# Kernel tuning notes

Measured on AMD Instinct MI355X. Metric: run time of the kernel, lower is better.

Reference implementation:

```python
import jax, jax.numpy as jnp
import numpy as np

NUM_HEADS = 16
LN_EPS = 1e-5

def _gelu(x):
    return jax.nn.gelu(x, approximate=False)  # torch default GELU is exact (erf)

def setup_inputs() -> dict:
    key = jax.random.key(0)
    ks = jax.random.split(key, 12)
    B, S, E = 2, 2048, 1024
    H = E // 2
    s = lambda fan_in: 1.0 / np.sqrt(fan_in)
    inp = {
        "x": jax.random.normal(ks[0], (B, S, E), jnp.float32),
        "Wq": jax.random.normal(ks[1], (E, E), jnp.float32) * s(E),
        "bq": jnp.zeros((E,), jnp.float32),
        "Wk": jax.random.normal(ks[2], (E, E), jnp.float32) * s(E),
        "bk": jnp.zeros((E,), jnp.float32),
        "Wv": jax.random.normal(ks[3], (E, E), jnp.float32) * s(E),
        "bv": jnp.zeros((E,), jnp.float32),
        "Wo": jax.random.normal(ks[4], (E, E), jnp.float32) * s(E),
        "bo": jnp.zeros((E,), jnp.float32),
        "dp_w1": jax.random.normal(ks[5], (E, H), jnp.float32) * s(E),
        "dp_b1": jnp.zeros((H,), jnp.float32),
        "ln_g": jnp.ones((H,), jnp.float32),
        "ln_b": jnp.zeros((H,), jnp.float32),
        "dp_w2": jax.random.normal(ks[6], (H, 1), jnp.float32) * s(H),
        "dp_b2": jnp.zeros((1,), jnp.float32),
        "g_w1": jax.random.normal(ks[7], (1, 16), jnp.float32),
        "g_b1": jnp.zeros((16,), jnp.float32),
        "g_w2": jax.random.normal(ks[8], (16, 1), jnp.float32) * s(16),
        "g_b2": jnp.zeros((1,), jnp.float32),
    }
    return inp


def reference(x, Wq, bq, Wk, bk, Wv, bv, Wo, bo,
              dp_w1, dp_b1, ln_g, ln_b, dp_w2, dp_b2,
              g_w1, g_b1, g_w2, g_b2):
    B, S, E = x.shape
    Hn = NUM_HEADS
    Dh = E // Hn
    scale = Dh ** -0.5

    Q = (x @ Wq + bq).reshape(B, S, Hn, Dh)
    K = (x @ Wk + bk).reshape(B, S, Hn, Dh)
    V = (x @ Wv + bv).reshape(B, S, Hn, Dh)

    # (B, H, q, k)
    logits = jnp.einsum('bqhd,bkhd->bhqk', Q, K) * scale
    causal = jnp.tril(jnp.ones((S, S), bool))
    logits = jnp.where(causal, logits, -jnp.inf)
    attn = jax.nn.softmax(logits, axis=-1)

    # drift probe: Linear -> LayerNorm -> GELU -> Linear, squeeze -> (B, S)
    h = x @ dp_w1 + dp_b1
    mu = h.mean(-1, keepdims=True)
    var = ((h - mu) ** 2).mean(-1, keepdims=True)
    h = (h - mu) / jnp.sqrt(var + LN_EPS) * ln_g + ln_b
    drift = (_gelu(h) @ dp_w2 + dp_b2)[..., 0]

    # drift_to_gate: Linear(1,16) -> GELU -> Linear(16,1) -> Tanh -> (B, S)
    g = _gelu(drift[..., None] * g_w1[0] + g_b1)
    gate = jnp.tanh(g @ g_w2 + g_b2)[..., 0]  # (B, S), indexed by key position

    gated = attn * gate[:, None, None, :]  # dropout p=0 -> identity
    out = jnp.einsum('bhqk,bkhd->bqhd', gated, V).reshape(B, S, E)
    return out @ Wo + bo
```

## Files before the change

### kernel.cpp

```cpp
#include <hip/hip_runtime.h>
#include <math.h>
#include <stdint.h>

#define B_   2
#define S_   2048
#define E_   1024
#define NH   16
#define DH   64
#define HID  512
#define NCAT 3584
#define MTOK 4096

typedef unsigned short ushort_t;
typedef short  s16x8  __attribute__((ext_vector_type(8)));
typedef unsigned short us4 __attribute__((ext_vector_type(4)));
typedef float  f32x4  __attribute__((ext_vector_type(4)));

static constexpr float LN_EPS    = 1e-5f;
static constexpr float SCALE     = 0.125f;
static constexpr float INV_SQRT2 = 0.70710678118654752440f;

__device__ __forceinline__ float gelu_exact(float v) {
    return 0.5f * v * (1.0f + erff(v * INV_SQRT2));
}

__device__ __forceinline__ ushort_t f2bf(float f) {
    unsigned int u = __float_as_uint(f);
    unsigned int r = u + 0x7fffu + ((u >> 16) & 1u);
    return (ushort_t)(r >> 16);
}
__device__ __forceinline__ float bf2f(ushort_t s) {
    return __uint_as_float(((unsigned int)s) << 16);
}

__device__ __forceinline__ void stage16(const void* g, void* ldsbase) {
#if __has_builtin(__builtin_amdgcn_global_load_lds)
    __builtin_amdgcn_global_load_lds(
        (const __attribute__((address_space(1))) void*)g,
        (__attribute__((address_space(3))) void*)ldsbase, 16, 0, 0);
#else
    ((uint4*)ldsbase)[threadIdx.x & 63] = *(const uint4*)g;
#endif
}

__device__ __forceinline__ void xcd_swizzle(int gx, int gy, int& bx, int& by) {
    const int T = gx * gy;
    const int lin = blockIdx.y * gx + blockIdx.x;
    const int work = (lin & 7) * (T >> 3) + (lin >> 3);
    bx = work % gx;
    by = work / gx;
}

__global__ __launch_bounds__(256) void preproc_kernel(
    const float* __restrict__ x,
    const float* __restrict__ Wq, const float* __restrict__ Wk,
    const float* __restrict__ Wv, const float* __restrict__ Wo,
    const float* __restrict__ dpw1,
    const float* __restrict__ bq, const float* __restrict__ bk,
    const float* __restrict__ bv, const float* __restrict__ b1,
    ushort_t* __restrict__ xh, ushort_t* __restrict__ xl,
    ushort_t* __restrict__ bth, ushort_t* __restrict__ btl,
    ushort_t* __restrict__ woth, ushort_t* __restrict__ wotl,
    float* __restrict__ bcat)
{
    __shared__ float tile[32][33];
    int bid = blockIdx.x;
    const int t = threadIdx.x;

    if (bid < 1024) {
        int base = bid * 1024 + t;
        #pragma unroll
        for (int it = 0; it < 4; ++it) {
            int i = base + it * 256;
            float4 v = ((const float4*)x)[i];
            float vv[4] = {v.x, v.y, v.z, v.w};
            us4 h, l;
            #pragma unroll
            for (int j = 0; j < 4; ++j) {
                ushort_t hh = f2bf(vv[j]);
                h[j] = hh;
                l[j] = f2bf(vv[j] - bf2f(hh));
            }
            *(us4*)&xh[(size_t)i * 4] = h;
            *(us4*)&xl[(size_t)i * 4] = l;
        }
        return;
    }
    bid -= 1024;
    if (bid < 4608) {
        const float* W; ushort_t *th, *tl; int N, kx, ny;
        if (bid < 1024)      { W = Wq;   th = bth;                        tl = btl;                        N = 1024; kx = bid & 31; ny = bid >> 5; }
        else if (bid < 2048) { W = Wk;   th = bth + (size_t)1024 * E_;    tl = btl + (size_t)1024 * E_;    N = 1024; kx = (bid - 1024) & 31; ny = (bid - 1024) >> 5; }
        else if (bid < 3072) { W = Wv;   th = bth + (size_t)2048 * E_;    tl = btl + (size_t)2048 * E_;    N = 1024; kx = (bid - 2048) & 31; ny = (bid - 2048) >> 5; }
        else if (bid < 4096) { W = Wo;   th = woth;                       tl = wotl;                       N = 1024; kx = (bid - 3072) & 31; ny = (bid - 3072) >> 5; }
        else                 { W = dpw1; th = bth + (size_t)3072 * E_;    tl = btl + (size_t)3072 * E_;    N = 512;  kx = (bid - 4096) & 31; ny = (bid - 4096) >> 5; }

        const int k0 = kx * 32, n0 = ny * 32;
        const int r = t >> 3, c4 = (t & 7) * 4;
        float4 v = *(const float4*)&W[(size_t)(k0 + r) * N + n0 + c4];
        tile[r][c4 + 0] = v.x; tile[r][c4 + 1] = v.y;
        tile[r][c4 + 2] = v.z; tile[r][c4 + 3] = v.w;
        __syncthreads();
        us4 h, l;
        #pragma unroll
        for (int i = 0; i < 4; ++i) {
            float xv = tile[c4 + i][r];
            ushort_t hh = f2bf(xv);
            h[i] = hh;
            l[i] = f2bf(xv - bf2f(hh));
        }
        *(us4*)&th[(size_t)(n0 + r) * E_ + k0 + c4] = h;
        *(us4*)&tl[(size_t)(n0 + r) * E_ + k0 + c4] = l;
        return;
    }
    bid -= 4608;
    int i = bid * 256 + t;
    if (i >= NCAT) return;
    float v;
    if      (i < 1024) v = bq[i];
    else if (i < 2048) v = bk[i - 1024];
    else if (i < 3072) v = bv[i - 2048];
    else               v = b1[i - 3072];
    bcat[i] = v;
}

struct GemmCtx {
    int lane, w, wr, wc;
};

__device__ __forceinline__ void gemm_core(
    const ushort_t* __restrict__ Ah, const ushort_t* __restrict__ Al,
    const ushort_t* __restrict__ Bh, const ushort_t* __restrict__ Bl,
    int row0, int col0, int Kd,
    ushort_t* Ahs, ushort_t* Als, ushort_t* Bhs, ushort_t* Bls,
    f32x4 (&acc)[4][4], const GemmCtx& cx)
{
    const int lr = cx.lane >> 2;
    const int lc = (cx.lane & 3) * 8;

    for (int k0 = 0; k0 < Kd; k0 += 32) {
        #pragma unroll
        for (int ii = 0; ii < 2; ++ii) {
            const int r0 = (cx.w * 2 + ii) * 16;
            const size_t ga = (size_t)(row0 + r0 + lr) * Kd + k0 + lc;
            const size_t gb = (size_t)(col0 + r0 + lr) * Kd + k0 + lc;
            stage16(Ah + ga, &Ahs[r0 * 32]);
            stage16(Al + ga, &Als[r0 * 32]);
            stage16(Bh + gb, &Bhs[r0 * 32]);
            stage16(Bl + gb, &Bls[r0 * 32]);
        }
        __syncthreads();

        const int rA = cx.wr * 64 + (cx.lane & 15);
        const int rB = cx.wc * 64 + (cx.lane & 15);
        const int kq = (cx.lane >> 4) * 8;
        s16x8 fah[4], fal[4], fbh[4], fbl[4];
        #pragma unroll
        for (int i = 0; i < 4; ++i) {
            fah[i] = *(const s16x8*)&Ahs[(rA + i * 16) * 32 + kq];
            fal[i] = *(const s16x8*)&Als[(rA + i * 16) * 32 + kq];
            fbh[i] = *(const s16x8*)&Bhs[(rB + i * 16) * 32 + kq];
            fbl[i] = *(const s16x8*)&Bls[(rB + i * 16) * 32 + kq];
        }
        __builtin_amdgcn_s_setprio(1);
        #pragma unroll
        for (int i = 0; i < 4; ++i)
            #pragma unroll
            for (int j = 0; j < 4; ++j) {
                acc[i][j] = __builtin_amdgcn_mfma_f32_16x16x32_bf16(fah[i], fbh[j], acc[i][j], 0, 0, 0);
                acc[i][j] = __builtin_amdgcn_mfma_f32_16x16x32_bf16(fah[i], fbl[j], acc[i][j], 0, 0, 0);
                acc[i][j] = __builtin_amdgcn_mfma_f32_16x16x32_bf16(fal[i], fbh[j], acc[i][j], 0, 0, 0);
            }
        __builtin_amdgcn_s_setprio(0);
        __syncthreads();
    }
}

__global__ __launch_bounds__(256) void mfma_gemm_qkvh_kernel(
    const ushort_t* __restrict__ Ah, const ushort_t* __restrict__ Al,
    const ushort_t* __restrict__ Bh, const ushort_t* __restrict__ Bl,
    const float* __restrict__ bias,
    ushort_t* __restrict__ Qh, ushort_t* __restrict__ Ql,
    ushort_t* __restrict__ Kh, ushort_t* __restrict__ Kl,
    float* __restrict__ v32, float* __restrict__ h32)
{
    __shared__ __align__(16) ushort_t Ahs[128 * 32];
    __shared__ __align__(16) ushort_t Als[128 * 32];
    __shared__ __align__(16) ushort_t Bhs[128 * 32];
    __shared__ __align__(16) ushort_t Bls[128 * 32];

    int bx, by;
    xcd_swizzle(28, 32, bx, by);
    const int row0 = by * 128, col0 = bx * 128;

    GemmCtx cx;
    cx.lane = threadIdx.x & 63;
    cx.w    = threadIdx.x >> 6;
    cx.wr   = cx.w >> 1; cx.wc = cx.w & 1;

    f32x4 acc[4][4] = {};
    gemm_core(Ah, Al, Bh, Bl, row0, col0, E_, Ahs, Als, Bhs, Bls, acc, cx);

    const int crow = row0 + cx.wr * 64 + ((cx.lane >> 4) * 4);
    const int ccol0 = col0 + cx.wc * 64 + (cx.lane & 15);

    #pragma unroll
    for (int j = 0; j < 4; ++j) {
        const int gcol = ccol0 + j * 16;
        const float bv = bias[gcol];
        #pragma unroll
        for (int i = 0; i < 4; ++i)
            #pragma unroll
            for (int r = 0; r < 4; ++r) {
                const int row = crow + i * 16 + r;
                float val = acc[i][j][r] + bv;
                if (gcol < 1024) {
                    val *= SCALE;
                    ushort_t hi = f2bf(val);
                    Qh[(size_t)row * 1024 + gcol] = hi;
                    Ql[(size_t)row * 1024 + gcol] = f2bf(val - bf2f(hi));
                } else if (gcol < 2048) {
                    ushort_t hi = f2bf(val);
                    Kh[(size_t)row * 1024 + gcol - 1024] = hi;
                    Kl[(size_t)row * 1024 + gcol - 1024] = f2bf(val - bf2f(hi));
                } else if (gcol < 3072) {
                    v32[(size_t)row * 1024 + gcol - 2048] = val;
                } else {
                    h32[(size_t)row * 512 + gcol - 3072] = val;
                }
            }
    }
}

__global__ __launch_bounds__(256) void mfma_gemm_kernel(
    const ushort_t* __restrict__ Ah, const ushort_t* __restrict__ Al,
    const ushort_t* __restrict__ Bh, const ushort_t* __restrict__ Bl,
    const float* __restrict__ bias,
    float* __restrict__ C, int N, int Kd)
{
    __shared__ __align__(16) ushort_t Ahs[128 * 32];
    __shared__ __align__(16) ushort_t Als[128 * 32];
    __shared__ __align__(16) ushort_t Bhs[128 * 32];
    __shared__ __align__(16) ushort_t Bls[128 * 32];

    int bx, by;
    xcd_swizzle(gridDim.x, gridDim.y, bx, by);
    const int row0 = by * 128, col0 = bx * 128;

    GemmCtx cx;
    cx.lane = threadIdx.x & 63;
    cx.w    = threadIdx.x >> 6;
    cx.wr   = cx.w >> 1; cx.wc = cx.w & 1;

    f32x4 acc[4][4] = {};
    gemm_core(Ah, Al, Bh, Bl, row0, col0, Kd, Ahs, Als, Bhs, Bls, acc, cx);

    const int crow = row0 + cx.wr * 64 + ((cx.lane >> 4) * 4);
    const int ccol = col0 + cx.wc * 64 + (cx.lane & 15);
    #pragma unroll
    for (int j = 0; j < 4; ++j) {
        const float bv = bias[ccol + j * 16];
        #pragma unroll
        for (int i = 0; i < 4; ++i)
            #pragma unroll
            for (int r = 0; r < 4; ++r)
                C[(size_t)(crow + i * 16 + r) * N + ccol + j * 16] = acc[i][j][r] + bv;
    }
}

__global__ __launch_bounds__(256) void ln_gate_kernel(
    const float* __restrict__ h32,
    const float* __restrict__ lng, const float* __restrict__ lnb,
    const float* __restrict__ w2,  const float* __restrict__ b2,
    const float* __restrict__ gw1, const float* __restrict__ gb1,
    const float* __restrict__ gw2, const float* __restrict__ gb2,
    float* __restrict__ gate)
{
    const int row  = blockIdx.x * 4 + (threadIdx.x >> 6);
    const int lane = threadIdx.x & 63;
    const float* h = h32 + (size_t)row * 512;

    float4 a = *(const float4*)&h[lane * 4];
    float4 b = *(const float4*)&h[256 + lane * 4];
    float va[8] = {a.x, a.y, a.z, a.w, b.x, b.y, b.z, b.w};

    float sum = 0.f, sq = 0.f;
    #pragma unroll
    for (int j = 0; j < 8; ++j) { sum += va[j]; sq += va[j] * va[j]; }
    #pragma unroll
    for (int o = 1; o < 64; o <<= 1) {
        sum += __shfl_xor(sum, o);
        sq  += __shfl_xor(sq,  o);
    }
    const float mu  = sum * (1.f / HID);
    const float inv = 1.f / sqrtf(sq * (1.f / HID) - mu * mu + LN_EPS);

    float4 g0 = *(const float4*)&lng[lane * 4];
    float4 g1 = *(const float4*)&lng[256 + lane * 4];
    float4 o0 = *(const float4*)&lnb[lane * 4];
    float4 o1 = *(const float4*)&lnb[256 + lane * 4];
    float4 w0 = *(const float4*)&w2[lane * 4];
    float4 w1 = *(const float4*)&w2[256 + lane * 4];
    float gg[8] = {g0.x, g0.y, g0.z, g0.w, g1.x, g1.y, g1.z, g1.w};
    float bb[8] = {o0.x, o0.y, o0.z, o0.w, o1.x, o1.y, o1.z, o1.w};
    float ww[8] = {w0.x, w0.y, w0.z, w0.w, w1.x, w1.y, w1.z, w1.w};

    float part = 0.f;
    #pragma unroll
    for (int j = 0; j < 8; ++j) {
        float nx = (va[j] - mu) * inv * gg[j] + bb[j];
        part += gelu_exact(nx) * ww[j];
    }
    #pragma unroll
    for (int o = 1; o < 64; o <<= 1) part += __shfl_xor(part, o);

    if (lane == 0) {
        float drift = part + b2[0];
        float gacc = gb2[0];
        #pragma unroll
        for (int i = 0; i < 16; ++i) {
            float tt = fmaf(drift, gw1[i], gb1[i]);
            gacc = fmaf(gelu_exact(tt), gw2[i], gacc);
        }
        gate[row] = tanhf(gacc);
    }
}

__global__ __launch_bounds__(256) void v_transpose_kernel(
    const float* __restrict__ v32, const float* __restrict__ gate,
    ushort_t* __restrict__ Vth, ushort_t* __restrict__ Vtl)
{
    __shared__ float T[64 * 68];
    const int kt = blockIdx.x, bh = blockIdx.y;
    const int b = bh >> 4, h = bh & 15;
    const int tid = threadIdx.x;

    #pragma unroll
    for (int it = 0; it < 4; ++it) {
        int idx = tid + it * 256;
        int tokr = idx >> 4, f4 = idx & 15;
        int tok = b * S_ + kt * 64 + tokr;
        float g = gate[tok];
        float4 v = *(const float4*)&v32[(size_t)tok * 1024 + h * 64 + f4 * 4];
        T[(f4 * 4 + 0) * 68 + tokr] = v.x * g;
        T[(f4 * 4 + 1) * 68 + tokr] = v.y * g;
        T[(f4 * 4 + 2) * 68 + tokr] = v.z * g;
        T[(f4 * 4 + 3) * 68 + tokr] = v.w * g;
    }
    __syncthreads();

    const int d = tid >> 2, t0 = (tid & 3) * 16;
    const size_t obase = (size_t)bh * 64 * S_ + (size_t)d * S_ + kt * 64 + t0;
    s16x8 h8[2], l8[2];
    #pragma unroll
    for (int u = 0; u < 16; ++u) {
        float f = T[d * 68 + t0 + u];
        ushort_t hh = f2bf(f);
        h8[u >> 3][u & 7] = (short)hh;
        l8[u >> 3][u & 7] = (short)f2bf(f - bf2f(hh));
    }
    *(s16x8*)&Vth[obase]     = h8[0];
    *(s16x8*)&Vth[obase + 8] = h8[1];
    *(s16x8*)&Vtl[obase]     = l8[0];
    *(s16x8*)&Vtl[obase + 8] = l8[1];
}

__global__ __launch_bounds__(512, 4) void attn_mfma_kernel(
    const ushort_t* __restrict__ Qh, const ushort_t* __restrict__ Ql,
    const ushort_t* __restrict__ Kh, const ushort_t* __restrict__ Kl,
    const ushort_t* __restrict__ Vth, const ushort_t* __restrict__ Vtl,
    ushort_t* __restrict__ ch, ushort_t* __restrict__ cl)
{
    __shared__ __align__(16) ushort_t Khs[64 * 72], Kls[64 * 72];
    __shared__ __align__(16) ushort_t Vhs[64 * 72], Vls[64 * 72];
    __shared__ __align__(16) unsigned int Ph[8 * 16 * 32];
    __shared__ __align__(16) unsigned int Pl[8 * 16 * 32];

    const int tid  = threadIdx.x;
    const int lane = tid & 63;
    const int w    = tid >> 6;
    const int g    = lane >> 4;
    const int c    = lane & 15;

    const int lin  = blockIdx.y * 16 + blockIdx.x;
    const int work = (lin & 7) * 64 + (lin >> 3);
    const int bh   = work >> 4;
    const int qt   = 15 - (work & 15);
    const int b    = bh >> 4, h = bh & 15;
    const int q0   = qt * 128;

    const size_t qkb = (size_t)b * S_ * 1024 + h * 64;
    const size_t vtb = (size_t)bh * 64 * S_;

    const int qwave = q0 + w * 16;

    const size_t qrow = qkb + (size_t)(qwave + c) * 1024;
    s16x8 qfh[2], qfl[2];
    qfh[0] = *(const s16x8*)&Qh[qrow + g * 8];
    qfh[1] = *(const s16x8*)&Qh[qrow + 32 + g * 8];
    qfl[0] = *(const s16x8*)&Ql[qrow + g * 8];
    qfl[1] = *(const s16x8*)&Ql[qrow + 32 + g * 8];

    f32x4 o4[4] = {};
    float m = -INFINITY, l = 0.f;

    #define PIDX(c_, kp_) ((w << 9) + ((c_) << 5) + ((kp_) ^ (((c_) & 7) << 2)))

    const int srow = tid >> 3, ssl = tid & 7;

    s16x8 pkh, pkl, pvh, pvl;
    pkh = *(const s16x8*)&Kh [qkb + (size_t)srow * 1024 + ssl * 8];
    pkl = *(const s16x8*)&Kl [qkb + (size_t)srow * 1024 + ssl * 8];
    pvh = *(const s16x8*)&Vth[vtb + (size_t)srow * S_ + ssl * 8];
    pvl = *(const s16x8*)&Vtl[vtb + (size_t)srow * S_ + ssl * 8];

    const int ktmax = 2 * qt + 1;

    for (int kt = 0; kt <= ktmax; ++kt) {
        const int k0 = kt * 64;
        *(s16x8*)&Khs[srow * 72 + ssl * 8] = pkh;
        *(s16x8*)&Kls[srow * 72 + ssl * 8] = pkl;
        *(s16x8*)&Vhs[srow * 72 + ssl * 8] = pvh;
        *(s16x8*)&Vls[srow * 72 + ssl * 8] = pvl;
        __syncthreads();

        if (kt < ktmax) {
            const int kn = k0 + 64;
            pkh = *(const s16x8*)&Kh [qkb + (size_t)(kn + srow) * 1024 + ssl * 8];
            pkl = *(const s16x8*)&Kl [qkb + (size_t)(kn + srow) * 1024 + ssl * 8];
            pvh = *(const s16x8*)&Vth[vtb + (size_t)srow * S_ + kn + ssl * 8];
            pvl = *(const s16x8*)&Vtl[vtb + (size_t)srow * S_ + kn + ssl * 8];
        }

        if (k0 <= qwave + 15) {
            f32x4 s4[4] = {};
            __builtin_amdgcn_s_setprio(1);
            #pragma unroll
            for (int j = 0; j < 4; ++j)
                #pragma unroll
                for (int ks = 0; ks < 2; ++ks) {
                    s16x8 kfh = *(const s16x8*)&Khs[(c + j * 16) * 72 + ks * 32 + g * 8];
                    s16x8 kfl = *(const s16x8*)&Kls[(c + j * 16) * 72 + ks * 32 + g * 8];
                    s4[j] = __builtin_amdgcn_mfma_f32_16x16x32_bf16(kfh, qfh[ks], s4[j], 0, 0, 0);
                    s4[j] = __builtin_amdgcn_mfma_f32_16x16x32_bf16(kfh, qfl[ks], s4[j], 0, 0, 0);
                    s4[j] = __builtin_amdgcn_mfma_f32_16x16x32_bf16(kfl, qfh[ks], s4[j], 0, 0, 0);
                }
            __builtin_amdgcn_s_setprio(0);

            if (k0 + 63 > qwave) {
                #pragma unroll
                for (int j = 0; j < 4; ++j)
                    #pragma unroll
                    for (int r = 0; r < 4; ++r)
                        if (k0 + j * 16 + g * 4 + r > qwave + c)
                            s4[j][r] = -INFINITY;
            }

            float pmax = -INFINITY;
            #pragma unroll
            for (int j = 0; j < 4; ++j)
                #pragma unroll
                for (int r = 0; r < 4; ++r) pmax = fmaxf(pmax, s4[j][r]);
            pmax = fmaxf(pmax, __shfl_xor(pmax, 16));
            pmax = fmaxf(pmax, __shfl_xor(pmax, 32));

            const bool nomax = __all(pmax <= m);
            const float mn = nomax ? m : fmaxf(m, pmax);

            float ps = 0.f;
            #pragma unroll
            for (int j = 0; j < 4; ++j)
                #pragma unroll
                for (int r = 0; r < 4; ++r) {
                    float p = __expf(s4[j][r] - mn);
                    s4[j][r] = p;
                    ps += p;
                }
            ps += __shfl_xor(ps, 16);
            ps += __shfl_xor(ps, 32);

            if (nomax) {
                l += ps;
            } else {
                float corr = (m == -INFINITY) ? 0.f : __expf(m - mn);
                l = l * corr + ps;
                m = mn;
                #pragma unroll
                for (int r = 0; r < 4; ++r) {
                    int src = ((g << 4) | (g * 4 + r)) << 2;
                    float cr = __int_as_float(
                        __builtin_amdgcn_ds_bpermute(src, __float_as_int(corr)));
                    #pragma unroll
                    for (int j = 0; j < 4; ++j) o4[j][r] *= cr;
                }
            }

            #pragma unroll
            for (int j = 0; j < 4; ++j)
                #pragma unroll
                for (int p = 0; p < 2; ++p) {
                    float e  = s4[j][2 * p];
                    float od = s4[j][2 * p + 1];
                    unsigned int hi2, lo2;
                    asm volatile("v_cvt_pk_bf16_f32 %0, %1, %2"
                                 : "=v"(hi2) : "v"(e), "v"(od));
                    float ef = __uint_as_float(hi2 << 16);
                    float of = __uint_as_float(hi2 & 0xffff0000u);
                    float el = e - ef, ol = od - of;
                    asm volatile("v_cvt_pk_bf16_f32 %0, %1, %2"
                                 : "=v"(lo2) : "v"(el), "v"(ol));
                    const int kp = j * 8 + g * 2 + p;
                    Ph[PIDX(c, kp)] = hi2;
                    Pl[PIDX(c, kp)] = lo2;
                }
            asm volatile("s_waitcnt lgkmcnt(0)" ::: "memory");
            __builtin_amdgcn_sched_barrier(0);

            union U4 { uint4 u; s16x8 v; };
            s16x8 pah[2], pal[2];
            #pragma unroll
            for (int ks = 0; ks < 2; ++ks) {
                U4 a, bb;
                a.u  = *(const uint4*)&Ph[PIDX(c, ks * 16 + g * 4)];
                bb.u = *(const uint4*)&Pl[PIDX(c, ks * 16 + g * 4)];
                pah[ks] = a.v;
                pal[ks] = bb.v;
            }

            __builtin_amdgcn_s_setprio(1);
            #pragma unroll
            for (int j = 0; j < 4; ++j)
                #pragma unroll
                for (int ks = 0; ks < 2; ++ks) {
                    s16x8 vfh = *(const s16x8*)&Vhs[(c + j * 16) * 72 + ks * 32 + g * 8];
                    s16x8 vfl = *(const s16x8*)&Vls[(c + j * 16) * 72 + ks * 32 + g * 8];
                    o4[j] = __builtin_amdgcn_mfma_f32_16x16x32_bf16(pah[ks], vfh, o4[j], 0, 0, 0);
                    o4[j] = __builtin_amdgcn_mfma_f32_16x16x32_bf16(pah[ks], vfl, o4[j], 0, 0, 0);
                    o4[j] = __builtin_amdgcn_mfma_f32_16x16x32_bf16(pal[ks], vfh, o4[j], 0, 0, 0);
                }
            __builtin_amdgcn_s_setprio(0);
        }
        __syncthreads();
    }

    float inv[4];
    #pragma unroll
    for (int r = 0; r < 4; ++r) {
        int src = ((g << 4) | (g * 4 + r)) << 2;
        float lb = __int_as_float(
            __builtin_amdgcn_ds_bpermute(src, __float_as_int(l)));
        inv[r] = 1.f / lb;
    }
    #pragma unroll
    for (int j = 0; j < 4; ++j)
        #pragma unroll
        for (int r = 0; r < 4; ++r) {
            float val = o4[j][r] * inv[r];
            int tok = b * S_ + qwave + g * 4 + r;
            int col = h * 64 + c + j * 16;
            ushort_t hi = f2bf(val);
            ch[(size_t)tok * 1024 + col] = hi;
            cl[(size_t)tok * 1024 + col] = f2bf(val - bf2f(hi));
        }
    #undef PIDX
}

extern "C" void kernel_launch(void* const* d_in, const int* in_sizes, int n_in,
                              void* d_out, int out_size, void* d_ws, size_t ws_size,
                              hipStream_t stream)
{
    const float* x    = (const float*)d_in[0];
    const float* Wq   = (const float*)d_in[1];  const float* bq   = (const float*)d_in[2];
    const float* Wk   = (const float*)d_in[3];  const float* bk   = (const float*)d_in[4];
    const float* Wv   = (const float*)d_in[5];  const float* bv   = (const float*)d_in[6];
    const float* Wo   = (const float*)d_in[7];  const float* bo   = (const float*)d_in[8];
    const float* dpw1 = (const float*)d_in[9];  const float* dpb1 = (const float*)d_in[10];
    const float* lng  = (const float*)d_in[11]; const float* lnb  = (const float*)d_in[12];
    const float* dpw2 = (const float*)d_in[13]; const float* dpb2 = (const float*)d_in[14];
    const float* gw1  = (const float*)d_in[15]; const float* gb1  = (const float*)d_in[16];
    const float* gw2  = (const float*)d_in[17]; const float* gb2  = (const float*)d_in[18];
    float* out = (float*)d_out;

    float* ws   = (float*)d_ws;
    float* v32  = ws;
    float* h32  = v32 + (size_t)MTOK * E_;
    float* bcat = h32 + (size_t)MTOK * HID;
    float* gate = bcat + NCAT;
    ushort_t* bp   = (ushort_t*)(gate + MTOK);
    ushort_t* xh   = bp;
    ushort_t* xl   = xh  + (size_t)MTOK * E_;
    ushort_t* bth  = xl  + (size_t)MTOK * E_;
    ushort_t* btl  = bth + (size_t)NCAT * E_;
    ushort_t* woth = btl + (size_t)NCAT * E_;
    ushort_t* wotl = woth + (size_t)E_ * E_;
    ushort_t* Qhb  = wotl + (size_t)E_ * E_;
    ushort_t* Qlb  = Qhb + (size_t)MTOK * E_;
    ushort_t* Khb  = Qlb + (size_t)MTOK * E_;
    ushort_t* Klb  = Khb + (size_t)MTOK * E_;
    ushort_t* Vthb = Klb + (size_t)MTOK * E_;
    ushort_t* Vtlb = Vthb + (size_t)MTOK * E_;
    ushort_t* chb  = xh;
    ushort_t* clb  = xl;

    hipLaunchKernelGGL(preproc_kernel, dim3(5646), dim3(256), 0, stream,
                       x, Wq, Wk, Wv, Wo, dpw1, bq, bk, bv, dpb1,
                       xh, xl, bth, btl, woth, wotl, bcat);

    hipLaunchKernelGGL(mfma_gemm_qkvh_kernel, dim3(28, 32), dim3(256), 0, stream,
                       xh, xl, bth, btl, bcat, Qhb, Qlb, Khb, Klb, v32, h32);

    hipLaunchKernelGGL(ln_gate_kernel, dim3(MTOK / 4), dim3(256), 0, stream,
                       h32, lng, lnb, dpw2, dpb2, gw1, gb1, gw2, gb2, gate);
    hipLaunchKernelGGL(v_transpose_kernel, dim3(32, 32), dim3(256), 0, stream,
                       v32, gate, Vthb, Vtlb);

    hipLaunchKernelGGL(attn_mfma_kernel, dim3(S_ / 128, B_ * NH), dim3(512), 0, stream,
                       Qhb, Qlb, Khb, Klb, Vthb, Vtlb, chb, clb);

    hipLaunchKernelGGL(mfma_gemm_kernel, dim3(E_ / 128, MTOK / 128), dim3(256), 0, stream,
                       chb, clb, woth, wotl, bo, out, E_, E_);
}
```

Before: 396.2 us.

## Stage GEMM epilogues through LDS for vectorized stores and use 2D XCD swizzle

Result: slower. 406.9 us (+2.7%).

```diff
diff --git a/kernel.cpp b/kernel.cpp
--- a/kernel.cpp
+++ b/kernel.cpp
@@ -49,6 +49,14 @@
     const int work = (lin & 7) * (T >> 3) + (lin >> 3);
     bx = work % gx;
     by = work / gx;
+}
+
+__device__ __forceinline__ void xcd_swizzle2d(int gx, int gy, int& bx, int& by) {
+    const int hx = gx >> 1, hy = gy >> 2;
+    const int lin = blockIdx.y * gx + blockIdx.x;
+    const int xcd = lin & 7, wk = lin >> 3;
+    bx = (xcd & 1) * hx + wk % hx;
+    by = (xcd >> 1) * hy + wk / hx;
 }
 
 __global__ __launch_bounds__(256) void preproc_kernel(
@@ -176,6 +184,8 @@
     }
 }
 
+#define EPS_STRIDE 140
+
 __global__ __launch_bounds__(256) void mfma_gemm_qkvh_kernel(
     const ushort_t* __restrict__ Ah, const ushort_t* __restrict__ Al,
     const ushort_t* __restrict__ Bh, const ushort_t* __restrict__ Bl,
@@ -184,51 +194,90 @@
     ushort_t* __restrict__ Kh, ushort_t* __restrict__ Kl,
     float* __restrict__ v32, float* __restrict__ h32)
 {
-    __shared__ __align__(16) ushort_t Ahs[128 * 32];
-    __shared__ __align__(16) ushort_t Als[128 * 32];
-    __shared__ __align__(16) ushort_t Bhs[128 * 32];
-    __shared__ __align__(16) ushort_t Bls[128 * 32];
+    __shared__ __align__(16) unsigned int eps[64 * EPS_STRIDE];
+    ushort_t* const Ahs = (ushort_t*)eps;
+    ushort_t* const Als = (ushort_t*)eps + 4096;
+    ushort_t* const Bhs = (ushort_t*)eps + 8192;
+    ushort_t* const Bls = (ushort_t*)eps + 12288;
 
     int bx, by;
-    xcd_swizzle(28, 32, bx, by);
+    xcd_swizzle2d(28, 32, bx, by);
     const int row0 = by * 128, col0 = bx * 128;
+    const int region = bx >> 3;
 
     GemmCtx cx;
     cx.lane = threadIdx.x & 63;
     cx.w    = threadIdx.x >> 6;
     cx.wr   = cx.w >> 1; cx.wc = cx.w & 1;
+    const int tid = threadIdx.x;
+    const int g = cx.lane >> 4, c = cx.lane & 15;
 
     f32x4 acc[4][4] = {};
     gemm_core(Ah, Al, Bh, Bl, row0, col0, E_, Ahs, Als, Bhs, Bls, acc, cx);
 
-    const int crow = row0 + cx.wr * 64 + ((cx.lane >> 4) * 4);
-    const int ccol0 = col0 + cx.wc * 64 + (cx.lane & 15);
-
-    #pragma unroll
-    for (int j = 0; j < 4; ++j) {
-        const int gcol = ccol0 + j * 16;
-        const float bv = bias[gcol];
-        #pragma unroll
-        for (int i = 0; i < 4; ++i)
-            #pragma unroll
-            for (int r = 0; r < 4; ++r) {
-                const int row = crow + i * 16 + r;
-                float val = acc[i][j][r] + bv;
-                if (gcol < 1024) {
-                    val *= SCALE;
-                    ushort_t hi = f2bf(val);
-                    Qh[(size_t)row * 1024 + gcol] = hi;
-                    Ql[(size_t)row * 1024 + gcol] = f2bf(val - bf2f(hi));
-                } else if (gcol < 2048) {
-                    ushort_t hi = f2bf(val);
-                    Kh[(size_t)row * 1024 + gcol - 1024] = hi;
-                    Kl[(size_t)row * 1024 + gcol - 1024] = f2bf(val - bf2f(hi));
-                } else if (gcol < 3072) {
-                    v32[(size_t)row * 1024 + gcol - 2048] = val;
-                } else {
-                    h32[(size_t)row * 512 + gcol - 3072] = val;
-                }
-            }
+    #pragma unroll
+    for (int rp = 0; rp < 2; ++rp) {
+        if (cx.wr == rp) {
+            #pragma unroll
+            for (int j = 0; j < 4; ++j) {
+                const int gcol = col0 + cx.wc * 64 + j * 16 + c;
+                const float bv = bias[gcol];
+                #pragma unroll
+                for (int i = 0; i < 4; ++i)
+                    #pragma unroll
+                    for (int r = 0; r < 4; ++r) {
+                        float val = acc[i][j][r] + bv;
+                        unsigned int payload;
+                        if (region < 2) {
+                            if (region == 0) val *= SCALE;
+                            ushort_t hi = f2bf(val);
+                            ushort_t lo = f2bf(val - bf2f(hi));
+                            payload = (unsigned int)hi | ((unsigned int)lo << 16);
+                        } else {
+                            payload = __float_as_uint(val);
+                        }
+                        const int lrow = g * 4 + i * 16 + r;
+                        const int lcol = cx.wc * 64 + j * 16 + c;
+                        eps[lrow * EPS_STRIDE + lcol] = payload;
+                    }
+            }
+        }
+        __syncthreads();
+
+        const int lrow = tid >> 2, qq = tid & 3;
+        const int grow = row0 + rp * 64 + lrow;
+        unsigned int vv[32];
+        #pragma unroll
+        for (int k = 0; k < 8; ++k)
+            *(uint4*)&vv[k * 4] = *(const uint4*)&eps[lrow * EPS_STRIDE + qq * 32 + k * 4];
+
+        if (region < 2) {
+            unsigned int hw[16], lw[16];
+            #pragma unroll
+            for (int t2 = 0; t2 < 16; ++t2) {
+                hw[t2] = (vv[2 * t2] & 0xffffu) | (vv[2 * t2 + 1] << 16);
+                lw[t2] = (vv[2 * t2] >> 16) | (vv[2 * t2 + 1] & 0xffff0000u);
+            }
+            ushort_t* oh = (region == 0) ? Qh : Kh;
+            ushort_t* ol = (region == 0) ? Ql : Kl;
+            const size_t obase = (size_t)grow * 1024 + (col0 - region * 1024) + qq * 32;
+            #pragma unroll
+            for (int k = 0; k < 4; ++k) {
+                *(uint4*)((unsigned int*)&oh[obase] + k * 4) = *(uint4*)&hw[k * 4];
+                *(uint4*)((unsigned int*)&ol[obase] + k * 4) = *(uint4*)&lw[k * 4];
+            }
+        } else if (region == 2) {
+            const size_t obase = (size_t)grow * 1024 + (col0 - 2048) + qq * 32;
+            #pragma unroll
+            for (int k = 0; k < 8; ++k)
+                *(uint4*)((unsigned int*)&v32[obase] + k * 4) = *(uint4*)&vv[k * 4];
+        } else {
+            const size_t obase = (size_t)grow * 512 + (col0 - 3072) + qq * 32;
+            #pragma unroll
+            for (int k = 0; k < 8; ++k)
+                *(uint4*)((unsigned int*)&h32[obase] + k * 4) = *(uint4*)&vv[k * 4];
+        }
+        if (rp == 0) __syncthreads();
     }
 }
 
@@ -238,33 +287,55 @@
     const float* __restrict__ bias,
     float* __restrict__ C, int N, int Kd)
 {
-    __shared__ __align__(16) ushort_t Ahs[128 * 32];
-    __shared__ __align__(16) ushort_t Als[128 * 32];
-    __shared__ __align__(16) ushort_t Bhs[128 * 32];
-    __shared__ __align__(16) ushort_t Bls[128 * 32];
+    __shared__ __align__(16) unsigned int eps[64 * EPS_STRIDE];
+    ushort_t* const Ahs = (ushort_t*)eps;
+    ushort_t* const Als = (ushort_t*)eps + 4096;
+    ushort_t* const Bhs = (ushort_t*)eps + 8192;
+    ushort_t* const Bls = (ushort_t*)eps + 12288;
 
     int bx, by;
-    xcd_swizzle(gridDim.x, gridDim.y, bx, by);
+    xcd_swizzle2d(gridDim.x, gridDim.y, bx, by);
     const int row0 = by * 128, col0 = bx * 128;
 
     GemmCtx cx;
     cx.lane = threadIdx.x & 63;
     cx.w    = threadIdx.x >> 6;
     cx.wr   = cx.w >> 1; cx.wc = cx.w & 1;
+    const int tid = threadIdx.x;
+    const int g = cx.lane >> 4, c = cx.lane & 15;
 
     f32x4 acc[4][4] = {};
     gemm_core(Ah, Al, Bh, Bl, row0, col0, Kd, Ahs, Als, Bhs, Bls, acc, cx);
 
-    const int crow = row0 + cx.wr * 64 + ((cx.lane >> 4) * 4);
-    const int ccol = col0 + cx.wc * 64 + (cx.lane & 15);
-    #pragma unroll
-    for (int j = 0; j < 4; ++j) {
-        const float bv = bias[ccol + j * 16];
-        #pragma unroll
-        for (int i = 0; i < 4; ++i)
-            #pragma unroll
-            for (int r = 0; r < 4; ++r)
-                C[(size_t)(crow + i * 16 + r) * N + ccol + j * 16] = acc[i][j][r] + bv;
+    #pragma unroll
+    for (int rp = 0; rp < 2; ++rp) {
+        if (cx.wr == rp) {
+            #pragma unroll
+            for (int j = 0; j < 4; ++j) {
+                const float bv = bias[col0 + cx.wc * 64 + j * 16 + c];
+                #pragma unroll
+                for (int i = 0; i < 4; ++i)
+                    #pragma unroll
+                    for (int r = 0; r < 4; ++r) {
+                        const int lrow = g * 4 + i * 16 + r;
+                        const int lcol = cx.wc * 64 + j * 16 + c;
+                        eps[lrow * EPS_STRIDE + lcol] = __float_as_uint(acc[i][j][r] + bv);
+                    }
+            }
+        }
+        __syncthreads();
+
+        const int lrow = tid >> 2, qq = tid & 3;
+        const int grow = row0 + rp * 64 + lrow;
+        unsigned int vv[32];
+        #pragma unroll
+        for (int k = 0; k < 8; ++k)
+            *(uint4*)&vv[k * 4] = *(const uint4*)&eps[lrow * EPS_STRIDE + qq * 32 + k * 4];
+        const size_t obase = (size_t)grow * N + col0 + qq * 32;
+        #pragma unroll
+        for (int k = 0; k < 8; ++k)
+            *(uint4*)((unsigned int*)&C[obase] + k * 4) = *(uint4*)&vv[k * 4];
+        if (rp == 0) __syncthreads();
     }
 }
 
```
